# Kernel tuning notes

Hardware: AMD Instinct MI355X
Metric: run time of the kernel (lower is better)

The kernel has to match this reference:

```python
import jax, jax.numpy as jnp
import numpy as np
from jax import lax

# Key identity used: modulating ALL weights of output channel o by s_o (with no bias
# inside the modulated conv, as in the source where F.conv2d(..., bias=None)) is
# mathematically identical to a plain conv followed by per-(batch, out_channel)
# scaling of the output. This collapses the per-sample Python loop into one conv.

def _upsample2x(x):
    # nearest-neighbor x2, matching F.interpolate(scale_factor=2) default mode
    return jnp.repeat(jnp.repeat(x, 2, axis=2), 2, axis=3)

def _conv(x, w):
    return lax.conv_general_dilated(
        x, w, window_strides=(1, 1), padding=[(1, 1), (1, 1)],
        dimension_numbers=("NCHW", "OIHW", "NCHW"))

def _modconv(x, style, w, fc_w, fc_b):
    # style_fc: [B, style_dim] -> [B, out_ch]
    s = style @ fc_w.T + fc_b          # [B, O]
    y = _conv(x, w)                    # [B, O, H, W]
    return y * s[:, :, None, None]


def setup_inputs() -> dict:
    key = jax.random.key(0)
    ks = jax.random.split(key, 16)
    B, SD = 8, 512
    chans = [(512, 256), (256, 128), (128, 64), (64, 64), (64, 64)]
    inp = {
        "x": jax.random.normal(ks[0], (B, 512, 8, 8), jnp.float32),
        "style": jax.random.normal(ks[1], (B, SD), jnp.float32),
    }
    for i, (ci, co) in enumerate(chans, start=1):
        inp[f"w{i}"] = jax.random.normal(ks[2 * i], (co, ci, 3, 3), jnp.float32) * (1.0 / np.sqrt(ci * 9))
        inp[f"fw{i}"] = jax.random.normal(ks[2 * i + 1], (co, SD), jnp.float32) * (1.0 / np.sqrt(SD))
        inp[f"fb{i}"] = jnp.ones((co,), jnp.float32)
    inp["wf"] = jax.random.normal(ks[12], (3, 64, 3, 3), jnp.float32) * (1.0 / np.sqrt(64 * 9))
    inp["bf"] = jnp.zeros((3,), jnp.float32)
    return inp


def reference(x, style, w1, fw1, fb1, w2, fw2, fb2, w3, fw3, fb3,
              w4, fw4, fb4, w5, fw5, fb5, wf, bf):
    x = _upsample2x(x)
    x = jax.nn.relu(_modconv(x, style, w1, fw1, fb1))
    x = _upsample2x(x)
    x = jax.nn.relu(_modconv(x, style, w2, fw2, fb2))
    x = _upsample2x(x)
    x = jax.nn.relu(_modconv(x, style, w3, fw3, fb3))
    x = _upsample2x(x)
    x = jax.nn.relu(_modconv(x, style, w4, fw4, fb4))
    x = _upsample2x(x)
    x = jax.nn.relu(_modconv(x, style, w5, fw5, fb5))
    x = _conv(x, wf) + bf[None, :, None, None]
    return x
```

## Files before the change

### kernel.cpp

```cpp
#include <hip/hip_runtime.h>
#include <hip/hip_bf16.h>
#include <cstddef>

typedef __bf16 bf16x8 __attribute__((ext_vector_type(8)));
typedef float f32x4 __attribute__((ext_vector_type(4)));

__global__ void prep_all_kernel(const float* __restrict__ x, __hip_bfloat16* __restrict__ act0,
                                const float* __restrict__ w1, __hip_bfloat16* __restrict__ o1,
                                const float* __restrict__ w2, __hip_bfloat16* __restrict__ o2,
                                const float* __restrict__ w3, __hip_bfloat16* __restrict__ o3,
                                const float* __restrict__ w4, __hip_bfloat16* __restrict__ o4,
                                const float* __restrict__ w5, __hip_bfloat16* __restrict__ o5,
                                const float* __restrict__ wf, __hip_bfloat16* __restrict__ of,
                                const float* __restrict__ style,
                                const float* __restrict__ fw1, const float* __restrict__ fb1,
                                const float* __restrict__ fw2, const float* __restrict__ fb2,
                                const float* __restrict__ fw3, const float* __restrict__ fb3,
                                const float* __restrict__ fw4, const float* __restrict__ fb4,
                                const float* __restrict__ fw5, const float* __restrict__ fb5,
                                float* __restrict__ S) {
    const int blk = blockIdx.x;
    if (blk < 1024) {
        int t = blk * 256 + threadIdx.x;
        int c = t & 511; int rest = t >> 9;
        int w = rest & 7; rest >>= 3; int h = rest & 7; int b = rest >> 3;
        act0[t] = __float2bfloat16(x[((b * 512 + c) * 8 + h) * 8 + w]);
    } else if (blk < 12324) {
        int t = (blk - 1024) * 256 + threadIdx.x;
        if (t < 2752512) {
            const float* w; __hip_bfloat16* o; int CI, lgCICH, lgCO16;
            if      (t < 2097152) { w = w1; o = o1; CI = 512; lgCICH = 3; lgCO16 = 4; }
            else if (t < 2621440) { t -= 2097152; w = w2; o = o2; CI = 256; lgCICH = 2; lgCO16 = 3; }
            else                  { t -= 2621440; w = w3; o = o3; CI = 128; lgCICH = 1; lgCO16 = 2; }
            int j    = t & 7;
            int ln   = (t >> 3) & 63;
            int ch   = (t >> 9) & 1;
            int cich = (t >> 10) & ((1 << lgCICH) - 1);
            int co16 = (t >> (10 + lgCICH)) & ((1 << lgCO16) - 1);
            int tap  = (t >> (10 + lgCICH + lgCO16)) & 3;
            int cls  = (t >> (12 + lgCICH + lgCO16)) & 3;
            int co = co16 * 16 + (ln & 15);
            int ci = cich * 64 + ch * 32 + (ln >> 4) * 8 + j;
            int py = cls >> 1, px = cls & 1;
            int i = tap >> 1, jj = tap & 1;
            int r0 = i * (1 + py), rc = py ? (2 - i) : (1 + i);
            int c0 = jj * (1 + px), cc = px ? (2 - jj) : (1 + jj);
            const float* wb = w + ((size_t)co * CI + ci) * 9;
            float s = 0.f;
            for (int rr = 0; rr < rc; ++rr)
                for (int c2 = 0; c2 < cc; ++c2)
                    s += wb[(r0 + rr) * 3 + (c0 + c2)];
            o[t] = __float2bfloat16(s);
        } else if (t < 2883584) {
            int u = t - 2752512;
            const float* w; __hip_bfloat16* o;
            if (u < 65536) { w = w4; o = o4; }
            else           { u -= 65536; w = w5; o = o5; }
            int j   = u & 7;
            int ln  = (u >> 3) & 63;
            int ch  = (u >> 9) & 1;
            int nt  = (u >> 10) & 3;
            int tp  = (u >> 12) & 3;
            int cls = (u >> 14) & 3;
            int py = cls >> 1, px = cls & 1;
            int i = tp >> 1, jj = tp & 1;
            int co = nt * 16 + (ln & 15);
            int ci = ch * 32 + (ln >> 4) * 8 + j;
            int r0 = i * (1 + py), rc = py ? (2 - i) : (1 + i);
            int c0 = jj * (1 + px), cc = px ? (2 - jj) : (1 + jj);
            const float* wb = w + ((size_t)co * 64 + ci) * 9;
            float s = 0.f;
            for (int rr = 0; rr < rc; ++rr)
                for (int c2 = 0; c2 < cc; ++c2)
                    s += wb[(r0 + rr) * 3 + (c0 + c2)];
            o[u] = __float2bfloat16(s);
        } else if (t < 2892800) {
            int u = t - 2883584;
            int j  = u & 7;
            int ln = (u >> 3) & 63;
            int ch = (u >> 9) & 1;
            int tap = u >> 10;
            int rr = ln & 15, qq = ln >> 4;
            int ci = ch * 32 + qq * 8 + j;
            float v = (rr < 3) ? wf[((size_t)rr * 64 + ci) * 9 + tap] : 0.f;
            of[u] = __float2bfloat16(v);
        }
    } else {
        int wvid = (blk - 12324) * 4 + (threadIdx.x >> 6);
        int lane = threadIdx.x & 63;
        const float* fw; const float* fb; int lg, sOff, local;
        if      (wvid < 2048) { fw = fw1; fb = fb1; lg = 8; sOff = 0;    local = wvid; }
        else if (wvid < 3072) { fw = fw2; fb = fb2; lg = 7; sOff = 2048; local = wvid - 2048; }
        else if (wvid < 3584) { fw = fw3; fb = fb3; lg = 6; sOff = 3072; local = wvid - 3072; }
        else if (wvid < 4096) { fw = fw4; fb = fb4; lg = 6; sOff = 3584; local = wvid - 3584; }
        else                  { fw = fw5; fb = fb5; lg = 6; sOff = 4096; local = wvid - 4096; }
        int b = local >> lg, o = local & ((1 << lg) - 1);
        const float* sb = style + b * 512;
        const float* fwo = fw + (size_t)o * 512;
        float p = 0.f;
        #pragma unroll
        for (int k = lane; k < 512; k += 64) p += sb[k] * fwo[k];
        #pragma unroll
        for (int off = 32; off > 0; off >>= 1) p += __shfl_down(p, off);
        if (lane == 0) S[sOff + local] = p + fb[o];
    }
}

template <int CI, int CO, int HS, int WS>
__launch_bounds__(512)
__global__ void conv_partial_kernel(const __hip_bfloat16* __restrict__ actIn,
                                    const __hip_bfloat16* __restrict__ wpk,
                                    float* __restrict__ Part) {
    constexpr int HO = HS * 2, WO = WS * 2;
    constexpr size_t sliceN = (size_t)8 * HO * WO * CO;
    constexpr int CICH = CI / 64, CO16 = CO / 16;

    const int tid = threadIdx.x;
    const int lane = tid & 63, wv = tid >> 6;
    const int r = lane & 15, q = lane >> 4;
    const int rs = r >> 3, sc = r & 7;
    const int lane8 = lane * 8;
    const int cls = wv >> 1, half = wv & 1;
    const int py = cls >> 1, px = cls & 1;

    const int pw = WO / 16, ppb = (HO / 16) * pw;
    const int b = blockIdx.x / ppb;
    const int prest = blockIdx.x - b * ppb;
    const int ph = prest / pw, pwi = prest - ph * pw;
    const int oh0 = ph * 16, ow0 = pwi * 16;
    const int sh0 = oh0 >> 1, sw0 = ow0 >> 1;
    const int n0 = blockIdx.y * 64;
    const int cich = blockIdx.z;
    const int ciOff = cich * 64;

    __shared__ alignas(16) __hip_bfloat16 Tile[100 * 72];

    f32x4 acc[2][4];
    #pragma unroll
    for (int i = 0; i < 2; ++i)
        #pragma unroll
        for (int j = 0; j < 4; ++j) acc[i][j] = f32x4{0.f, 0.f, 0.f, 0.f};

    for (int i = tid; i < 800; i += 512) {
        int pix = i >> 3, koct = i & 7;
        int tr = pix / 10, tc2 = pix - tr * 10;
        int su = sh0 - 1 + tr, sv = sw0 - 1 + tc2;
        uint4 v = {0, 0, 0, 0};
        if (su >= 0 && su < HS && sv >= 0 && sv < WS)
            v = *(const uint4*)(actIn + ((size_t)((b * HS + su) * WS + sv) * CI + ciOff + koct * 8));
        *(uint4*)&Tile[pix * 72 + koct * 8] = v;
    }
    __syncthreads();

    bf16x8 bA[4][2], bB[4][2];

    auto loadB = [&](bf16x8 (&dst)[4][2], int tp) {
        #pragma unroll
        for (int nt = 0; nt < 4; ++nt) {
            const int co16g = (n0 >> 4) + nt;
            #pragma unroll
            for (int ch = 0; ch < 2; ++ch)
                dst[nt][ch] = *(const bf16x8*)(wpk +
                    ((size_t)((((cls * 4 + tp) * CO16 + co16g) * CICH + cich) * 2 + ch) << 9) + lane8);
        }
    };

    auto compute = [&](int tp, bf16x8 (&bfr)[4][2]) {
        const int i = tp >> 1, j = tp & 1;
        const int ro = i + py, co2 = j + px;
        int apix[2];
        #pragma unroll
        for (int mt = 0; mt < 2; ++mt)
            apix[mt] = (2 * (half * 2 + mt) + rs + ro) * 10 + (sc + co2);
        #pragma unroll
        for (int ch = 0; ch < 2; ++ch) {
            bf16x8 af[2];
            #pragma unroll
            for (int mt = 0; mt < 2; ++mt)
                af[mt] = *(const bf16x8*)&Tile[apix[mt] * 72 + ch * 32 + q * 8];
            #pragma unroll
            for (int mt = 0; mt < 2; ++mt)
                #pragma unroll
                for (int nt = 0; nt < 4; ++nt)
                    acc[mt][nt] = __builtin_amdgcn_mfma_f32_16x16x32_bf16(
                        af[mt], bfr[nt][ch], acc[mt][nt], 0, 0, 0);
        }
    };

    loadB(bA, 0);
    loadB(bB, 1);
    compute(0, bA);
    loadB(bA, 2);
    compute(1, bB);
    loadB(bB, 3);
    compute(2, bA);
    compute(3, bB);

    float* P = Part + (size_t)blockIdx.z * sliceN;
    #pragma unroll
    for (int mt = 0; mt < 2; ++mt) {
        #pragma unroll
        for (int t2 = 0; t2 < 4; ++t2) {
            const int m = q * 4 + t2;
            const int row = oh0 + 2 * (2 * (half * 2 + mt) + (m >> 3)) + py;
            const int col = ow0 + 2 * (m & 7) + px;
            const size_t obase = ((size_t)(b * HO + row) * WO + col) * CO + n0;
            #pragma unroll
            for (int nt = 0; nt < 4; ++nt)
                P[obase + nt * 16 + r] = acc[mt][nt][t2];
        }
    }
}

template <int KS, int CO, int HW>
__launch_bounds__(256)
__global__ void reduce_kernel(const float* __restrict__ Part, const float* __restrict__ S,
                              __hip_bfloat16* __restrict__ actOut) {
    constexpr size_t sliceN = (size_t)8 * HW * CO;
    size_t e = ((size_t)blockIdx.x * 256 + threadIdx.x) * 4;
    if (e >= sliceN) return;
    f32x4 sum = {0.f, 0.f, 0.f, 0.f};
    #pragma unroll
    for (int k = 0; k < KS; ++k) sum += *(const f32x4*)(Part + (size_t)k * sliceN + e);
    const int co = (int)(e & (CO - 1));
    const int b = (int)(e / ((size_t)HW * CO));
    const float* Sb = S + b * CO + co;
    union { ushort4 u; __hip_bfloat16 h[4]; } pack;
    #pragma unroll
    for (int j = 0; j < 4; ++j)
        pack.h[j] = __float2bfloat16(fmaxf(sum[j] * Sb[j], 0.f));
    *(ushort4*)((unsigned short*)actOut + e) = pack.u;
}

__launch_bounds__(256)
__global__ void conv_s3_kernel(const __hip_bfloat16* __restrict__ actIn,
                               const __hip_bfloat16* __restrict__ wpk,
                               const float* __restrict__ S,
                               __hip_bfloat16* __restrict__ actOut) {
    constexpr int HS = 32, WS = 32, CI = 128, CO16 = 4, CICH = 2;

    const int tid = threadIdx.x;
    const int lane = tid & 63, wv = tid >> 6;
    const int r = lane & 15, q = lane >> 4;
    const int rr2 = r >> 2, cc2 = r & 3;
    const int lane8 = lane * 8;
    const int py = wv >> 1, px = wv & 1;

    const int b = blockIdx.x >> 6;
    const int prest = blockIdx.x & 63;
    const int ph = prest >> 3, pwi = prest & 7;
    const int oh0 = ph * 8, ow0 = pwi * 8;
    const int sh0 = oh0 >> 1, sw0 = ow0 >> 1;

    __shared__ alignas(16) __hip_bfloat16 Tile[36 * 72];

    f32x4 acc[4];
    #pragma unroll
    for (int j = 0; j < 4; ++j) acc[j] = f32x4{0.f, 0.f, 0.f, 0.f};

    bf16x8 bA[4][2], bB[4][2];

    #pragma unroll 1
    for (int cich = 0; cich < CICH; ++cich) {
        if (cich) __syncthreads();
        for (int i = tid; i < 288; i += 256) {
            int pix = i >> 3, koct = i & 7;
            int tr = pix / 6, tc2 = pix - tr * 6;
            int su = sh0 - 1 + tr, sv = sw0 - 1 + tc2;
            uint4 v = {0, 0, 0, 0};
            if (su >= 0 && su < HS && sv >= 0 && sv < WS)
                v = *(const uint4*)(actIn +
                    ((size_t)((b * HS + su) * WS + sv) * CI + cich * 64 + koct * 8));
            *(uint4*)&Tile[pix * 72 + koct * 8] = v;
        }
        __syncthreads();

        auto loadB = [&](bf16x8 (&dst)[4][2], int tp) {
            #pragma unroll
            for (int nt = 0; nt < 4; ++nt)
                #pragma unroll
                for (int ch = 0; ch < 2; ++ch)
                    dst[nt][ch] = *(const bf16x8*)(wpk +
                        ((size_t)((((wv * 4 + tp) * CO16 + nt) * CICH + cich) * 2 + ch) << 9) + lane8);
        };

        auto compute = [&](int tp, bf16x8 (&bfr)[4][2]) {
            const int i = tp >> 1, j = tp & 1;
            const int apix = (rr2 + i + py) * 6 + (cc2 + j + px);
            #pragma unroll
            for (int ch = 0; ch < 2; ++ch) {
                bf16x8 af = *(const bf16x8*)&Tile[apix * 72 + ch * 32 + q * 8];
                #pragma unroll
                for (int nt = 0; nt < 4; ++nt)
                    acc[nt] = __builtin_amdgcn_mfma_f32_16x16x32_bf16(
                        af, bfr[nt][ch], acc[nt], 0, 0, 0);
            }
        };

        loadB(bA, 0);
        loadB(bB, 1);
        compute(0, bA);
        loadB(bA, 2);
        compute(1, bB);
        loadB(bB, 3);
        compute(2, bA);
        compute(3, bB);
    }

    float sv_[4];
    #pragma unroll
    for (int nt = 0; nt < 4; ++nt) sv_[nt] = S[b * 64 + nt * 16 + r];
    #pragma unroll
    for (int t2 = 0; t2 < 4; ++t2) {
        const int m = q * 4 + t2;
        const int row = oh0 + 2 * (m >> 2) + py;
        const int col = ow0 + 2 * (m & 3) + px;
        const size_t obase = ((size_t)(b * 64 + row) * 64 + col) * 64;
        #pragma unroll
        for (int nt = 0; nt < 4; ++nt)
            actOut[obase + nt * 16 + r] =
                __float2bfloat16(fmaxf(acc[nt][t2] * sv_[nt], 0.f));
    }
}

template <int HS, int WS>
__launch_bounds__(256)
__global__ void conv_patch_kernel(const __hip_bfloat16* __restrict__ actIn,
                                  const __hip_bfloat16* __restrict__ wpk,
                                  const float* __restrict__ S,
                                  __hip_bfloat16* __restrict__ actOut) {
    constexpr int HO = HS * 2, WO = WS * 2;

    const int tid = threadIdx.x;
    const int lane = tid & 63, wv = tid >> 6;
    const int r = lane & 15, q = lane >> 4;
    const int rs = r >> 3, sc = r & 7;
    const int lane8 = lane * 8;
    const int py = wv >> 1, px = wv & 1;

    const int pw = WO / 16, ppb = (HO / 16) * pw;
    const int b = blockIdx.x / ppb;
    const int prest = blockIdx.x - b * ppb;
    const int ph = prest / pw, pwi = prest - ph * pw;
    const int oh0 = ph * 16, ow0 = pwi * 16;
    const int sh0 = oh0 >> 1, sw0 = ow0 >> 1;

    __shared__ alignas(16) __hip_bfloat16 Tile[100 * 72];

    f32x4 acc[4][4];
    #pragma unroll
    for (int i = 0; i < 4; ++i)
        #pragma unroll
        for (int j = 0; j < 4; ++j) acc[i][j] = f32x4{0.f, 0.f, 0.f, 0.f};

    for (int i = tid; i < 800; i += 256) {
        int pix = i >> 3, koct = i & 7;
        int tr = pix / 10, tc2 = pix - tr * 10;
        int su = sh0 - 1 + tr, sv = sw0 - 1 + tc2;
        uint4 v = {0, 0, 0, 0};
        if (su >= 0 && su < HS && sv >= 0 && sv < WS)
            v = *(const uint4*)(actIn + ((size_t)((b * HS + su) * WS + sv) * 64 + koct * 8));
        *(uint4*)&Tile[pix * 72 + koct * 8] = v;
    }
    __syncthreads();

    const __hip_bfloat16* wcls = wpk + ((size_t)wv << 14);

    bf16x8 bA[4][2], bB[4][2];

    auto loadB = [&](bf16x8 (&dst)[4][2], int tp) {
        #pragma unroll
        for (int nt = 0; nt < 4; ++nt)
            #pragma unroll
            for (int ch = 0; ch < 2; ++ch)
                dst[nt][ch] = *(const bf16x8*)(wcls + (tp << 12) + ((nt * 2 + ch) << 9) + lane8);
    };

    auto compute = [&](int tp, bf16x8 (&bfr)[4][2]) {
        const int i = tp >> 1, j = tp & 1;
        const int ro = i + py, co2 = j + px;
        int apix[4];
        #pragma unroll
        for (int mt = 0; mt < 4; ++mt)
            apix[mt] = (2 * mt + rs + ro) * 10 + (sc + co2);
        #pragma unroll
        for (int ch = 0; ch < 2; ++ch) {
            bf16x8 af[4];
            #pragma unroll
            for (int mt = 0; mt < 4; ++mt)
                af[mt] = *(const bf16x8*)&Tile[apix[mt] * 72 + ch * 32 + q * 8];
            #pragma unroll
            for (int mt = 0; mt < 4; ++mt)
                #pragma unroll
                for (int nt = 0; nt < 4; ++nt)
                    acc[mt][nt] = __builtin_amdgcn_mfma_f32_16x16x32_bf16(
                        af[mt], bfr[nt][ch], acc[mt][nt], 0, 0, 0);
        }
    };

    loadB(bA, 0);
    loadB(bB, 1);
    compute(0, bA);
    loadB(bA, 2);
    compute(1, bB);
    loadB(bB, 3);
    compute(2, bA);
    compute(3, bB);

    float sv_[4];
    #pragma unroll
    for (int nt = 0; nt < 4; ++nt) sv_[nt] = S[b * 64 + nt * 16 + r];
    #pragma unroll
    for (int mt = 0; mt < 4; ++mt) {
        #pragma unroll
        for (int t2 = 0; t2 < 4; ++t2) {
            const int m = q * 4 + t2;
            const int row = oh0 + 4 * mt + 2 * (m >> 3) + py;
            const int col = ow0 + 2 * (m & 7) + px;
            const size_t obase = ((size_t)(b * HO + row) * WO + col) * 64;
            #pragma unroll
            for (int nt = 0; nt < 4; ++nt)
                actOut[obase + nt * 16 + r] =
                    __float2bfloat16(fmaxf(acc[mt][nt][t2] * sv_[nt], 0.f));
        }
    }
}

__launch_bounds__(256)
__global__ void conv_final_kernel(const __hip_bfloat16* __restrict__ actIn,
                                  const __hip_bfloat16* __restrict__ wpkF,
                                  const float* __restrict__ bias,
                                  float* __restrict__ out) {
    constexpr int HO = 256, WO = 256;
    const int tid = threadIdx.x, lane = tid & 63, wv = tid >> 6;
    const int r = lane & 15, q = lane >> 4;
    const int lane8 = lane * 8;

    const int ppb = 32 * 16;
    const int b = blockIdx.x / ppb;
    const int prest = blockIdx.x - b * ppb;
    const int ph = prest >> 4, pwi = prest & 15;
    const int oh0 = ph * 8, ow0 = pwi * 16;

    __shared__ alignas(16) __hip_bfloat16 Tile[10 * 18 * 72];

    for (int i = tid; i < 1440; i += 256) {
        int pix = i >> 3, koct = i & 7;
        int tr = pix / 18, tc2 = pix - tr * 18;
        int u = oh0 - 1 + tr, v = ow0 - 1 + tc2;
        uint4 val = {0, 0, 0, 0};
        if (u >= 0 && u < HO && v >= 0 && v < WO)
            val = *(const uint4*)(actIn + ((size_t)((b * HO + u) * WO + v) * 64 + koct * 8));
        *(uint4*)&Tile[pix * 72 + koct * 8] = val;
    }
    __syncthreads();

    f32x4 acc[2];
    acc[0] = f32x4{0.f, 0.f, 0.f, 0.f};
    acc[1] = f32x4{0.f, 0.f, 0.f, 0.f};

    #pragma unroll 1
    for (int tap = 0; tap < 9; ++tap) {
        const int dyv = tap / 3;
        const int dxv = tap - dyv * 3;
        const int tc = r + dxv;
        int apix[2];
        #pragma unroll
        for (int mt = 0; mt < 2; ++mt)
            apix[mt] = (wv * 2 + mt + dyv) * 18 + tc;
        #pragma unroll
        for (int ch = 0; ch < 2; ++ch) {
            bf16x8 bfr = *(const bf16x8*)(wpkF + ((tap * 2 + ch) << 9) + lane8);
            #pragma unroll
            for (int mt = 0; mt < 2; ++mt) {
                bf16x8 af = *(const bf16x8*)&Tile[apix[mt] * 72 + ch * 32 + q * 8];
                acc[mt] = __builtin_amdgcn_mfma_f32_16x16x32_bf16(af, bfr, acc[mt], 0, 0, 0);
            }
        }
    }

    if (r < 3) {
        const float bs = bias[r];
        #pragma unroll
        for (int mt = 0; mt < 2; ++mt) {
            const int prow = wv * 2 + mt;
            #pragma unroll
            for (int t2 = 0; t2 < 4; ++t2) {
                const int pcol = q * 4 + t2;
                out[((size_t)(b * 3 + r) << 16) + (oh0 + prow) * 256 + ow0 + pcol] =
                    acc[mt][t2] + bs;
            }
        }
    }
}

extern "C" void kernel_launch(void* const* d_in, const int* in_sizes, int n_in,
                              void* d_out, int out_size, void* d_ws, size_t ws_size,
                              hipStream_t stream) {
    const float* x    = (const float*)d_in[0];
    const float* sty  = (const float*)d_in[1];
    const float* w1   = (const float*)d_in[2];
    const float* fw1  = (const float*)d_in[3];
    const float* fb1  = (const float*)d_in[4];
    const float* w2   = (const float*)d_in[5];
    const float* fw2  = (const float*)d_in[6];
    const float* fb2  = (const float*)d_in[7];
    const float* w3   = (const float*)d_in[8];
    const float* fw3  = (const float*)d_in[9];
    const float* fb3  = (const float*)d_in[10];
    const float* w4   = (const float*)d_in[11];
    const float* fw4  = (const float*)d_in[12];
    const float* fb4  = (const float*)d_in[13];
    const float* w5   = (const float*)d_in[14];
    const float* fw5  = (const float*)d_in[15];
    const float* fb5  = (const float*)d_in[16];
    const float* wf   = (const float*)d_in[17];
    const float* bf   = (const float*)d_in[18];
    float* out = (float*)d_out;

    char* ws = (char*)d_ws;
    size_t off = 0;
    auto alloc = [&](size_t bytes) {
        char* p = ws + off;
        off += (bytes + 255) & ~(size_t)255;
        return p;
    };
    float* S1 = (float*)alloc(8 * 256 * 4);
    float* S2 = (float*)alloc(8 * 128 * 4);
    float* S3 = (float*)alloc(8 * 64 * 4);
    float* S4 = (float*)alloc(8 * 64 * 4);
    float* S5 = (float*)alloc(8 * 64 * 4);
    __hip_bfloat16* act0 = (__hip_bfloat16*)alloc((size_t)262144 * 2);
    __hip_bfloat16* act1 = (__hip_bfloat16*)alloc((size_t)524288 * 2);
    __hip_bfloat16* act2 = (__hip_bfloat16*)alloc((size_t)1048576 * 2);
    __hip_bfloat16* act3 = (__hip_bfloat16*)alloc((size_t)2097152 * 2);
    __hip_bfloat16* act4 = (__hip_bfloat16*)alloc((size_t)8388608 * 2);
    __hip_bfloat16* act5 = (__hip_bfloat16*)alloc((size_t)33554432 * 2);
    __hip_bfloat16* wt1  = (__hip_bfloat16*)alloc((size_t)2097152 * 2);
    __hip_bfloat16* wt2  = (__hip_bfloat16*)alloc((size_t)524288 * 2);
    __hip_bfloat16* wt3  = (__hip_bfloat16*)alloc((size_t)131072 * 2);
    __hip_bfloat16* wt4  = (__hip_bfloat16*)alloc((size_t)65536 * 2);
    __hip_bfloat16* wt5  = (__hip_bfloat16*)alloc((size_t)65536 * 2);
    __hip_bfloat16* wtF  = (__hip_bfloat16*)alloc((size_t)9 * 16 * 64 * 2);
    if (off > ws_size) return;

    float* Part = (float*)act5;

    prep_all_kernel<<<13476, 256, 0, stream>>>(x, act0,
                                               w1, wt1, w2, wt2, w3, wt3,
                                               w4, wt4, w5, wt5, wf, wtF,
                                               sty, fw1, fb1, fw2, fb2, fw3, fb3,
                                               fw4, fb4, fw5, fb5, S1);

    conv_partial_kernel<512, 256, 8, 8><<<dim3(8, 4, 8), 512, 0, stream>>>(act0, wt1, Part);
    reduce_kernel<8, 256, 256><<<512, 256, 0, stream>>>(Part, S1, act1);
    conv_partial_kernel<256, 128, 16, 16><<<dim3(32, 2, 4), 512, 0, stream>>>(act1, wt2, Part);
    reduce_kernel<4, 128, 1024><<<1024, 256, 0, stream>>>(Part, S2, act2);

    conv_s3_kernel<<<512, 256, 0, stream>>>(act2, wt3, S3, act3);

    conv_patch_kernel<64, 64><<<dim3(512), 256, 0, stream>>>(act3, wt4, S4, act4);
    conv_patch_kernel<128, 128><<<dim3(2048), 256, 0, stream>>>(act4, wt5, S5, act5);

    conv_final_kernel<<<4096, 256, 0, stream>>>(act5, wtF, bf, out);
}
```

Before: 205.9 us.

## Fuse fifth modulated conv with final conv through shared-memory tile

Replaces the separate layer-5 conv and final 3-channel conv kernels with one kernel. Each block computes a 16x16 output patch plus a one-pixel halo of the layer-5 activation, using the subpixel (upsample-folded) weight classes, and writes it to LDS. It then runs the final conv from LDS, so the 256x256x64 bf16 activation never round-trips through global memory and one launch is removed. In exchange, the halo pixels of layer 5 are recomputed by neighbouring blocks, and the larger 512-thread block with a bigger LDS footprint may reduce occupancy.

```diff
diff --git a/kernel.cpp b/kernel.cpp
--- a/kernel.cpp
+++ b/kernel.cpp
@@ -426,38 +426,130 @@
     }
 }
 
-__launch_bounds__(256)
-__global__ void conv_final_kernel(const __hip_bfloat16* __restrict__ actIn,
-                                  const __hip_bfloat16* __restrict__ wpkF,
-                                  const float* __restrict__ bias,
-                                  float* __restrict__ out) {
-    constexpr int HO = 256, WO = 256;
-    const int tid = threadIdx.x, lane = tid & 63, wv = tid >> 6;
+__launch_bounds__(512)
+__global__ void conv_s5f_kernel(const __hip_bfloat16* __restrict__ actIn,
+                                const __hip_bfloat16* __restrict__ wpk5,
+                                const __hip_bfloat16* __restrict__ wpkF,
+                                const float* __restrict__ S,
+                                const float* __restrict__ bias,
+                                float* __restrict__ out) {
+    constexpr int HS = 128, WS = 128;
+
+    const int tid = threadIdx.x;
+    const int lane = tid & 63, wv = tid >> 6;
     const int r = lane & 15, q = lane >> 4;
     const int lane8 = lane * 8;
-
-    const int ppb = 32 * 16;
-    const int b = blockIdx.x / ppb;
-    const int prest = blockIdx.x - b * ppb;
-    const int ph = prest >> 4, pwi = prest & 15;
-    const int oh0 = ph * 8, ow0 = pwi * 16;
-
-    __shared__ alignas(16) __hip_bfloat16 Tile[10 * 18 * 72];
-
-    for (int i = tid; i < 1440; i += 256) {
+    const int cls = wv >> 1, half = wv & 1;
+    const int py = cls >> 1, px = cls & 1;
+
+    const int bid = blockIdx.x;
+    const int b = bid >> 8;
+    const int rest = bid & 255;
+    const int oh0 = (rest >> 4) * 16, ow0 = (rest & 15) * 16;
+    const int sh0 = oh0 >> 1, sw0 = ow0 >> 1;
+
+    __shared__ alignas(16) __hip_bfloat16 Lds[18 * 18 * 72];
+    __hip_bfloat16* TileA = Lds;
+
+    for (int i = tid; i < 800; i += 512) {
         int pix = i >> 3, koct = i & 7;
-        int tr = pix / 18, tc2 = pix - tr * 18;
-        int u = oh0 - 1 + tr, v = ow0 - 1 + tc2;
-        uint4 val = {0, 0, 0, 0};
-        if (u >= 0 && u < HO && v >= 0 && v < WO)
-            val = *(const uint4*)(actIn + ((size_t)((b * HO + u) * WO + v) * 64 + koct * 8));
-        *(uint4*)&Tile[pix * 72 + koct * 8] = val;
+        int tr = pix / 10, tc2 = pix - tr * 10;
+        int su = sh0 - 1 + tr, sv = sw0 - 1 + tc2;
+        uint4 v = {0, 0, 0, 0};
+        if (su >= 0 && su < HS && sv >= 0 && sv < WS)
+            v = *(const uint4*)(actIn + ((size_t)((b * HS + su) * WS + sv) * 64 + koct * 8));
+        *(uint4*)&TileA[pix * 72 + koct * 8] = v;
     }
     __syncthreads();
 
-    f32x4 acc[2];
-    acc[0] = f32x4{0.f, 0.f, 0.f, 0.f};
-    acc[1] = f32x4{0.f, 0.f, 0.f, 0.f};
+    f32x4 acc[3][4];
+    #pragma unroll
+    for (int i = 0; i < 3; ++i)
+        #pragma unroll
+        for (int j = 0; j < 4; ++j) acc[i][j] = f32x4{0.f, 0.f, 0.f, 0.f};
+
+    int jrA[3], jcA[3];
+    #pragma unroll
+    for (int mt = 0; mt < 3; ++mt) {
+        int pm = half * 48 + mt * 16 + r;
+        pm = pm > 80 ? 80 : pm;
+        jrA[mt] = (pm * 57) >> 9;
+        jcA[mt] = pm - jrA[mt] * 9;
+    }
+
+    const __hip_bfloat16* wcls = wpk5 + ((size_t)cls << 14);
+
+    bf16x8 bA[4][2], bB[4][2];
+
+    auto loadB = [&](bf16x8 (&dst)[4][2], int tp) {
+        #pragma unroll
+        for (int nt = 0; nt < 4; ++nt)
+            #pragma unroll
+            for (int ch = 0; ch < 2; ++ch)
+                dst[nt][ch] = *(const bf16x8*)(wcls + (tp << 12) + ((nt * 2 + ch) << 9) + lane8);
+    };
+
+    auto compute = [&](int tp, bf16x8 (&bfr)[4][2]) {
+        const int i = tp >> 1, j = tp & 1;
+        int apix[3];
+        #pragma unroll
+        for (int mt = 0; mt < 3; ++mt)
+            apix[mt] = (jrA[mt] + i) * 10 + (jcA[mt] + j);
+        #pragma unroll
+        for (int ch = 0; ch < 2; ++ch) {
+            bf16x8 af[3];
+            #pragma unroll
+            for (int mt = 0; mt < 3; ++mt)
+                af[mt] = *(const bf16x8*)&TileA[apix[mt] * 72 + ch * 32 + q * 8];
+            #pragma unroll
+            for (int mt = 0; mt < 3; ++mt)
+                #pragma unroll
+                for (int nt = 0; nt < 4; ++nt)
+                    acc[mt][nt] = __builtin_amdgcn_mfma_f32_16x16x32_bf16(
+                        af[mt], bfr[nt][ch], acc[mt][nt], 0, 0, 0);
+        }
+    };
+
+    loadB(bA, 0);
+    loadB(bB, 1);
+    compute(0, bA);
+    loadB(bA, 2);
+    compute(1, bB);
+    loadB(bB, 3);
+    compute(2, bA);
+    compute(3, bB);
+
+    float sv_[4];
+    #pragma unroll
+    for (int nt = 0; nt < 4; ++nt) sv_[nt] = S[b * 64 + nt * 16 + r];
+
+    __syncthreads();
+
+    #pragma unroll
+    for (int mt = 0; mt < 3; ++mt) {
+        #pragma unroll
+        for (int t2 = 0; t2 < 4; ++t2) {
+            const int m = half * 48 + mt * 16 + q * 4 + t2;
+            if (m < 81) {
+                const int jr = (m * 57) >> 9;
+                const int jc = m - jr * 9;
+                const int p  = py ? (oh0 - 1 + 2 * jr) : (oh0 + 2 * jr);
+                const int pc = px ? (ow0 - 1 + 2 * jc) : (ow0 + 2 * jc);
+                const bool valid = (p >= 0) && (p < 256) && (pc >= 0) && (pc < 256);
+                const int dpx = (2 * jr + 1 - py) * 18 + (2 * jc + 1 - px);
+                #pragma unroll
+                for (int nt = 0; nt < 4; ++nt) {
+                    float v = valid ? fmaxf(acc[mt][nt][t2] * sv_[nt], 0.f) : 0.f;
+                    Lds[dpx * 72 + nt * 16 + r] = __float2bfloat16(v);
+                }
+            }
+        }
+    }
+    __syncthreads();
+
+    f32x4 acc2[2];
+    acc2[0] = f32x4{0.f, 0.f, 0.f, 0.f};
+    acc2[1] = f32x4{0.f, 0.f, 0.f, 0.f};
 
     #pragma unroll 1
     for (int tap = 0; tap < 9; ++tap) {
@@ -473,8 +565,8 @@
             bf16x8 bfr = *(const bf16x8*)(wpkF + ((tap * 2 + ch) << 9) + lane8);
             #pragma unroll
             for (int mt = 0; mt < 2; ++mt) {
-                bf16x8 af = *(const bf16x8*)&Tile[apix[mt] * 72 + ch * 32 + q * 8];
-                acc[mt] = __builtin_amdgcn_mfma_f32_16x16x32_bf16(af, bfr, acc[mt], 0, 0, 0);
+                bf16x8 af = *(const bf16x8*)&Lds[apix[mt] * 72 + ch * 32 + q * 8];
+                acc2[mt] = __builtin_amdgcn_mfma_f32_16x16x32_bf16(af, bfr, acc2[mt], 0, 0, 0);
             }
         }
     }
@@ -483,13 +575,11 @@
         const float bs = bias[r];
         #pragma unroll
         for (int mt = 0; mt < 2; ++mt) {
-            const int prow = wv * 2 + mt;
-            #pragma unroll
-            for (int t2 = 0; t2 < 4; ++t2) {
-                const int pcol = q * 4 + t2;
-                out[((size_t)(b * 3 + r) << 16) + (oh0 + prow) * 256 + ow0 + pcol] =
-                    acc[mt][t2] + bs;
-            }
+            const int prow = oh0 + wv * 2 + mt;
+            #pragma unroll
+            for (int t2 = 0; t2 < 4; ++t2)
+                out[((size_t)(b * 3 + r) << 16) + prow * 256 + ow0 + q * 4 + t2] =
+                    acc2[mt][t2] + bs;
         }
     }
 }
@@ -560,7 +650,6 @@
     conv_s3_kernel<<<512, 256, 0, stream>>>(act2, wt3, S3, act3);
 
     conv_patch_kernel<64, 64><<<dim3(512), 256, 0, stream>>>(act3, wt4, S4, act4);
-    conv_patch_kernel<128, 128><<<dim3(2048), 256, 0, stream>>>(act4, wt5, S5, act5);
-
-    conv_final_kernel<<<4096, 256, 0, stream>>>(act5, wtF, bf, out);
+
+    conv_s5f_kernel<<<2048, 512, 0, stream>>>(act4, wt5, wtF, S5, bf, out);
 }
```

After: 197.1 us. 1.04x faster.
